# Kernel optimization log

Measured on AMD Instinct MI355X. Metric: run time of the kernel, lower is better.

## Reference

```python
import jax, jax.numpy as jnp
import numpy as np

B, N, N_IN, N_H = 8192, 16, 512, 256
NEG_ROUND = 1
MARGIN = 0.5
EPS = 1e-6  # torch F.pairwise_distance default eps


def setup_inputs() -> dict:
    key = jax.random.key(0)
    k0, k1, k2, k3 = jax.random.split(key, 4)
    seq1 = jax.random.normal(k0, (B, N, N_IN), dtype=jnp.float32)
    adj = jax.random.uniform(k1, (B, N, N), dtype=jnp.float32)
    # GCN linear (bias=False), xavier_uniform on [n_h, n_in] == same bound for [n_in, n_h]
    gx = float(np.sqrt(6.0 / (N_IN + N_H)))
    W_gcn = jax.random.uniform(k2, (N_IN, N_H), dtype=jnp.float32, minval=-gx, maxval=gx)
    b_gcn = jnp.zeros((N_H,), dtype=jnp.float32)  # Simple_GCN self.bias, init 0
    prelu_a = jnp.asarray(0.25, dtype=jnp.float32)  # nn.PReLU default
    bx = float(np.sqrt(6.0 / (N_H + N_H)))
    W_bil = jax.random.uniform(k3, (N_H, N_H), dtype=jnp.float32, minval=-bx, maxval=bx)
    b_bil = jnp.zeros((), dtype=jnp.float32)
    return {"seq1": seq1, "adj": adj, "W_gcn": W_gcn, "b_gcn": b_gcn,
            "prelu_a": prelu_a, "W_bil": W_bil, "b_bil": b_bil}


def reference(seq1, adj, W_gcn, b_gcn, prelu_a, W_bil, b_bil):
    # Simple_GCN: linear -> adjacency aggregate -> bias -> PReLU
    seq_fts = jnp.einsum('bnf,fh->bnh', seq1, W_gcn)           # [B,N,n_h]
    h1 = jnp.einsum('bnm,bmh->bnh', adj, seq_fts) + b_gcn      # bmm(adj, seq_fts)+bias
    h1 = jnp.where(h1 >= 0, h1, prelu_a * h1)                  # PReLU

    # avg readout over context nodes; last node is the target
    c = jnp.mean(h1[:, :-1, :], axis=1)                        # [B,n_h]
    h_mv = h1[:, -1, :]                                        # [B,n_h]

    def bilinear(x1, x2):  # nn.Bilinear(n_h, n_h, 1)
        return jnp.einsum('bi,ij,bj->b', x1, W_bil, x2)[:, None] + b_bil  # [B,1]

    scs = [bilinear(h_mv, c)]
    c_mi = c
    for _ in range(NEG_ROUND):  # fixed small loop, mirrors torch shift
        c_mi = jnp.concatenate([c_mi[-2:-1, :], c_mi[:-1, :]], axis=0)
        scs.append(bilinear(h_mv, c_mi))

    pos_dis = jnp.linalg.norm(h_mv - c + EPS, axis=-1)         # F.pairwise_distance
    neg_dis = jnp.linalg.norm(h_mv - c_mi + EPS, axis=-1)

    logits = jnp.concatenate(scs, axis=0)                      # [(1+NEG)*B, 1]
    # MarginRankingLoss(margin, reduction='none') with y=-1:
    # max(0, -y*(x1-x2)+margin) = max(0, (pos-neg)+margin)
    loss2 = jnp.maximum(0.0, (pos_dis - neg_dis) + MARGIN)     # [B]
    return (logits, loss2)
```

## Files before the change

kernel.cpp:

```cpp
#include <hip/hip_runtime.h>
#include <stdint.h>

typedef float f32x4 __attribute__((ext_vector_type(4)));
typedef __bf16 bfrag __attribute__((ext_vector_type(8)));
typedef unsigned short us4 __attribute__((ext_vector_type(4)));

__device__ __forceinline__ unsigned short f2bf(float f) {
  unsigned u = __float_as_uint(f);
  u += 0x7fff + ((u >> 16) & 1);
  return (unsigned short)(u >> 16);
}
__device__ __forceinline__ float bf2f(unsigned short s) {
  return __uint_as_float(((unsigned)s) << 16);
}

typedef __attribute__((address_space(3))) void lds_vp;
typedef __attribute__((address_space(1))) void gl_vp;
__device__ __forceinline__ void gload16(const void* g, void* l) {
  __builtin_amdgcn_global_load_lds((const gl_vp*)g, (lds_vp*)l, 16, 0, 0);
}

__global__ __launch_bounds__(256)
void conv_w_k(const float* __restrict__ Wg, const float* __restrict__ Wb,
              unsigned short* __restrict__ WgT, unsigned short* __restrict__ WbT) {
  int i = blockIdx.x * 256 + threadIdx.x;
  if (i < 512 * 256) { int k = i >> 8, c = i & 255; WgT[c * 512 + k] = f2bf(Wg[i]); }
  if (i < 256 * 256) { int k = i >> 8, c = i & 255; WbT[c * 256 + k] = f2bf(Wb[i]); }
}

__device__ __forceinline__ void stage1(const float* __restrict__ A,
                                       const unsigned short* __restrict__ Bt,
                                       char* buf, int tile, int kc, int t) {
#pragma unroll
  for (int i = 0; i < 4; i++) {
    int c = i * 512 + t;
    int row = c >> 4, s = c & 15;
    int sp = s ^ (row & 7);
    gload16(A + (size_t)(tile * 128 + row) * 512 + kc * 64 + sp * 4, buf + c * 16);
  }
#pragma unroll
  for (int i = 0; i < 4; i++) {
    int c = i * 512 + t;
    int col = c >> 3, s = c & 7;
    int sp = s ^ (col & 7);
    gload16(Bt + (size_t)col * 512 + kc * 64 + sp * 8, buf + 32768 + c * 16);
  }
}

__global__ __launch_bounds__(512)
void fused1_k(const float* __restrict__ A, const unsigned short* __restrict__ Bt,
              const float* __restrict__ adj, const float* __restrict__ b_gcn,
              const float* __restrict__ prelu_a,
              float* __restrict__ Cout, float* __restrict__ Hmv) {
  extern __shared__ __align__(16) char sm[];
  const int t = threadIdx.x;
  const int lane = t & 63;
  const int wid = t >> 6;
  const int wm = wid >> 2, wn = wid & 3;
  const int lrow = lane & 15, lgrp = lane >> 4;
  const int wg = blockIdx.x;

  const float pa = prelu_a[0];
  const f32x4 bg = *(const f32x4*)(b_gcn + lane * 4);

  stage1(A, Bt, sm, wg * 4, 0, t);

  for (int mt = 0; mt < 4; ++mt) {
    const int tile = wg * 4 + mt;
    f32x4 acc[4][4];
#pragma unroll
    for (int m = 0; m < 4; m++)
#pragma unroll
      for (int n = 0; n < 4; n++) acc[m][n] = (f32x4)0.0f;

    for (int kc = 0; kc < 8; ++kc) {
      char* cur = sm + (kc & 1) * 65536;
      if (!(mt == 3 && kc == 7)) {
        int nt = (kc < 7) ? tile : tile + 1;
        int nk = (kc < 7) ? kc + 1 : 0;
        stage1(A, Bt, sm + ((kc + 1) & 1) * 65536, nt, nk, t);
        asm volatile("s_waitcnt vmcnt(8)" ::: "memory");
      } else {
        asm volatile("s_waitcnt vmcnt(0)" ::: "memory");
      }
      __builtin_amdgcn_s_barrier();
      asm volatile("" ::: "memory");

#pragma unroll
      for (int kk = 0; kk < 2; kk++) {
        bfrag bfv[4];
#pragma unroll
        for (int n = 0; n < 4; n++) {
          int bcol = wn * 64 + n * 16 + lrow;
          int gs = (kk * 4 + lgrp) ^ (bcol & 7);
          bfv[n] = *(const bfrag*)(cur + 32768 + bcol * 128 + (gs << 4));
        }
#pragma unroll
        for (int m = 0; m < 4; m++) {
          int arow = wm * 64 + m * 16 + lrow;
          int s0 = (kk * 8 + lgrp * 2) ^ (arow & 7);
          int s1 = (kk * 8 + lgrp * 2 + 1) ^ (arow & 7);
          f32x4 lo = *(const f32x4*)(cur + arow * 256 + (s0 << 4));
          f32x4 hi = *(const f32x4*)(cur + arow * 256 + (s1 << 4));
          bfrag am;
          am[0] = (__bf16)lo.x; am[1] = (__bf16)lo.y; am[2] = (__bf16)lo.z; am[3] = (__bf16)lo.w;
          am[4] = (__bf16)hi.x; am[5] = (__bf16)hi.y; am[6] = (__bf16)hi.z; am[7] = (__bf16)hi.w;
#pragma unroll
          for (int n = 0; n < 4; n++)
            acc[m][n] = __builtin_amdgcn_mfma_f32_16x16x32_bf16(am, bfv[n], acc[m][n], 0, 0, 0);
        }
      }
      __builtin_amdgcn_s_barrier();
      asm volatile("" ::: "memory");
    }

    unsigned short* sf = (unsigned short*)(sm + 65536);
#pragma unroll
    for (int m = 0; m < 4; m++) {
      int row = wm * 64 + m * 16 + lgrp * 4;
#pragma unroll
      for (int n = 0; n < 4; n++) {
        int col = wn * 64 + n * 16 + lrow;
#pragma unroll
        for (int rr = 0; rr < 4; rr++)
          sf[(row + rr) * 256 + col] = f2bf(acc[m][n][rr]);
      }
    }
    asm volatile("s_waitcnt lgkmcnt(0)" ::: "memory");
    __builtin_amdgcn_s_barrier();
    asm volatile("" ::: "memory");

    f32x4 sfr[16];
#pragma unroll
    for (int mm = 0; mm < 16; mm++) {
      us4 q = *(const us4*)(sf + (wid * 16 + mm) * 256 + lane * 4);
      f32x4 v;
      v.x = bf2f(q.x); v.y = bf2f(q.y); v.z = bf2f(q.z); v.w = bf2f(q.w);
      sfr[mm] = v;
    }
    const int b = tile * 8 + wid;
    const float* adjb = adj + (size_t)b * 256;
    f32x4 cacc = (f32x4)0.0f;
    f32x4 hmv = (f32x4)0.0f;
#pragma unroll
    for (int n = 0; n < 16; n++) {
      f32x4 a4 = (f32x4)0.0f;
#pragma unroll
      for (int m = 0; m < 16; m++) a4 += adjb[n * 16 + m] * sfr[m];
      a4 += bg;
      f32x4 hv;
      hv.x = a4.x >= 0.f ? a4.x : pa * a4.x;
      hv.y = a4.y >= 0.f ? a4.y : pa * a4.y;
      hv.z = a4.z >= 0.f ? a4.z : pa * a4.z;
      hv.w = a4.w >= 0.f ? a4.w : pa * a4.w;
      if (n < 15) cacc += hv; else hmv = hv;
    }
    cacc *= (1.0f / 15.0f);
    *(f32x4*)(Cout + (size_t)b * 256 + lane * 4) = cacc;
    *(f32x4*)(Hmv + (size_t)b * 256 + lane * 4) = hmv;

    asm volatile("s_waitcnt lgkmcnt(0)" ::: "memory");
    __builtin_amdgcn_s_barrier();
    asm volatile("" ::: "memory");
  }
}

__device__ __forceinline__ void stage2(const float* __restrict__ A,
                                       const unsigned short* __restrict__ Bt,
                                       char* buf, int wg, int kc, int t) {
  {
    int c = t & 255;
    int row = c >> 3, s = c & 7;
    int sp = s ^ (((row & 3) << 1) | ((row >> 2) & 1));
    gload16(A + (size_t)(wg * 32 + row) * 256 + kc * 32 + sp * 4, buf + c * 16);
  }
#pragma unroll
  for (int i = 0; i < 2; i++) {
    int c = i * 512 + t;
    int col = c >> 2, s = c & 3;
    int sp = s ^ ((col ^ (col >> 2)) & 3);
    gload16(Bt + (size_t)col * 256 + kc * 32 + sp * 8, buf + 4096 + c * 16);
  }
}

__global__ __launch_bounds__(512)
void fused2_k(const float* __restrict__ A, const unsigned short* __restrict__ Bt,
              const float* __restrict__ C, const float* __restrict__ Hmv,
              const float* __restrict__ b_bil, float* __restrict__ out) {
  __shared__ __align__(16) char sm2[40960];
  const int t = threadIdx.x;
  const int lane = t & 63;
  const int wid = t >> 6;
  const int wm = wid >> 2, wn = wid & 3;
  const int lrow = lane & 15, lgrp = lane >> 4;
  const int wg = blockIdx.x;

  f32x4 acc[4];
#pragma unroll
  for (int n = 0; n < 4; n++) acc[n] = (f32x4)0.0f;

  stage2(A, Bt, sm2, wg, 0, t);

  for (int kc = 0; kc < 8; ++kc) {
    char* cur = sm2 + (kc & 1) * 20480;
    if (kc + 1 < 8) {
      stage2(A, Bt, sm2 + ((kc + 1) & 1) * 20480, wg, kc + 1, t);
      asm volatile("s_waitcnt vmcnt(3)" ::: "memory");
    } else {
      asm volatile("s_waitcnt vmcnt(0)" ::: "memory");
    }
    __builtin_amdgcn_s_barrier();
    asm volatile("" ::: "memory");

    bfrag bf[4];
#pragma unroll
    for (int n = 0; n < 4; n++) {
      int bcol = wn * 64 + n * 16 + lrow;
      int sB = (bcol ^ (bcol >> 2)) & 3;
      bf[n] = *(const bfrag*)(cur + 4096 + bcol * 64 + ((lgrp ^ sB) << 4));
    }
    {
      int arow = wm * 16 + lrow;
      int sw = ((arow & 3) << 1) | ((arow >> 2) & 1);
      f32x4 lo = *(const f32x4*)(cur + arow * 128 + (((lgrp * 2) ^ sw) << 4));
      f32x4 hi = *(const f32x4*)(cur + arow * 128 + (((lgrp * 2 + 1) ^ sw) << 4));
      bfrag am;
      am[0] = (__bf16)lo.x; am[1] = (__bf16)lo.y; am[2] = (__bf16)lo.z; am[3] = (__bf16)lo.w;
      am[4] = (__bf16)hi.x; am[5] = (__bf16)hi.y; am[6] = (__bf16)hi.z; am[7] = (__bf16)hi.w;
#pragma unroll
      for (int n = 0; n < 4; n++)
        acc[n] = __builtin_amdgcn_mfma_f32_16x16x32_bf16(am, bf[n], acc[n], 0, 0, 0);
    }
    __builtin_amdgcn_s_barrier();
    asm volatile("" ::: "memory");
  }

  float* sf = (float*)sm2;
  {
    int row = wm * 16 + lgrp * 4;
#pragma unroll
    for (int n = 0; n < 4; n++) {
      int col = wn * 64 + n * 16 + lrow;
#pragma unroll
      for (int rr = 0; rr < 4; rr++)
        sf[(row + rr) * 256 + col] = acc[n][rr];
    }
  }
  asm volatile("s_waitcnt lgkmcnt(0)" ::: "memory");
  __builtin_amdgcn_s_barrier();
  asm volatile("" ::: "memory");

  const float bb = b_bil[0];
#pragma unroll
  for (int r = 0; r < 4; ++r) {
    const int row = wid * 4 + r;
    const int b = wg * 32 + row;
    const int bp = (b == 0) ? 8190 : (b - 1);
    f32x4 tv = *(const f32x4*)(sf + row * 256 + lane * 4);
    f32x4 cv = *(const f32x4*)(C + (size_t)b * 256 + lane * 4);
    f32x4 cp = *(const f32x4*)(C + (size_t)bp * 256 + lane * 4);
    f32x4 hv = *(const f32x4*)(Hmv + (size_t)b * 256 + lane * 4);
    f32x4 d0 = hv - cv + 1e-6f;
    f32x4 d1 = hv - cp + 1e-6f;
    float s0 = tv.x * cv.x + tv.y * cv.y + tv.z * cv.z + tv.w * cv.w;
    float s1 = tv.x * cp.x + tv.y * cp.y + tv.z * cp.z + tv.w * cp.w;
    float p = d0.x * d0.x + d0.y * d0.y + d0.z * d0.z + d0.w * d0.w;
    float q = d1.x * d1.x + d1.y * d1.y + d1.z * d1.z + d1.w * d1.w;
#pragma unroll
    for (int m = 1; m < 64; m <<= 1) {
      s0 += __shfl_xor(s0, m, 64);
      s1 += __shfl_xor(s1, m, 64);
      p  += __shfl_xor(p, m, 64);
      q  += __shfl_xor(q, m, 64);
    }
    if (lane == 0) {
      out[b] = s0 + bb;
      out[8192 + b] = s1 + bb;
      out[16384 + b] = fmaxf(0.0f, sqrtf(p) - sqrtf(q) + 0.5f);
    }
  }
}

extern "C" void kernel_launch(void* const* d_in, const int* in_sizes, int n_in,
                              void* d_out, int out_size, void* d_ws, size_t ws_size,
                              hipStream_t stream) {
  (void)in_sizes; (void)n_in; (void)out_size; (void)ws_size;
  const float* seq1 = (const float*)d_in[0];
  const float* adj  = (const float*)d_in[1];
  const float* Wg   = (const float*)d_in[2];
  const float* bg   = (const float*)d_in[3];
  const float* pa   = (const float*)d_in[4];
  const float* Wb   = (const float*)d_in[5];
  const float* bb   = (const float*)d_in[6];
  float* out = (float*)d_out;
  char* ws = (char*)d_ws;

  unsigned short* WgT = (unsigned short*)(ws);
  unsigned short* WbT = (unsigned short*)(ws + 262144);
  float* C   = (float*)(ws + 524288);
  float* HMV = (float*)(ws + 524288 + 8388608);

  (void)hipFuncSetAttribute((const void*)fused1_k,
                            hipFuncAttributeMaxDynamicSharedMemorySize, 131072);

  hipLaunchKernelGGL(conv_w_k, dim3(512), dim3(256), 0, stream, Wg, Wb, WgT, WbT);
  hipLaunchKernelGGL(fused1_k, dim3(256), dim3(512), 131072, stream,
                     seq1, WgT, adj, bg, pa, C, HMV);
  hipLaunchKernelGGL(fused2_k, dim3(256), dim3(512), 0, stream,
                     HMV, WbT, C, HMV, bb, out);
}
```

Baseline: 104.8 us.

## Replace LDS-staged persistent GEMM with direct global loads and more blocks

The first fused kernel no longer stages seq1 and the transposed GCN weight through double-buffered LDS with async global-to-LDS loads. Each wave now reads its MFMA fragments straight from global memory. The kernel processes one 128-row tile per block over 1024 blocks instead of looping over four tiles per block, and uses only a 64KB static LDS buffer for the aggregation step. The goal is higher occupancy and less barrier and LDS traffic, relying on caches for operand reuse. The cost is that the global fragment loads are strided and uncoalesced, and the copy-compute overlap of the explicit pipeline is lost.

```diff
diff --git a/kernel.cpp b/kernel.cpp
--- a/kernel.cpp
+++ b/kernel.cpp
@@ -28,31 +28,12 @@
   if (i < 256 * 256) { int k = i >> 8, c = i & 255; WbT[c * 256 + k] = f2bf(Wb[i]); }
 }
 
-__device__ __forceinline__ void stage1(const float* __restrict__ A,
-                                       const unsigned short* __restrict__ Bt,
-                                       char* buf, int tile, int kc, int t) {
-#pragma unroll
-  for (int i = 0; i < 4; i++) {
-    int c = i * 512 + t;
-    int row = c >> 4, s = c & 15;
-    int sp = s ^ (row & 7);
-    gload16(A + (size_t)(tile * 128 + row) * 512 + kc * 64 + sp * 4, buf + c * 16);
-  }
-#pragma unroll
-  for (int i = 0; i < 4; i++) {
-    int c = i * 512 + t;
-    int col = c >> 3, s = c & 7;
-    int sp = s ^ (col & 7);
-    gload16(Bt + (size_t)col * 512 + kc * 64 + sp * 8, buf + 32768 + c * 16);
-  }
-}
-
-__global__ __launch_bounds__(512)
+__global__ __launch_bounds__(512, 4)
 void fused1_k(const float* __restrict__ A, const unsigned short* __restrict__ Bt,
               const float* __restrict__ adj, const float* __restrict__ b_gcn,
               const float* __restrict__ prelu_a,
               float* __restrict__ Cout, float* __restrict__ Hmv) {
-  extern __shared__ __align__(16) char sm[];
+  __shared__ unsigned short sf[128 * 256];
   const int t = threadIdx.x;
   const int lane = t & 63;
   const int wid = t >> 6;
@@ -60,109 +41,81 @@
   const int lrow = lane & 15, lgrp = lane >> 4;
   const int wg = blockIdx.x;
 
+  const float* a0 = A + (size_t)(wg * 128 + wm * 64 + lrow) * 512 + lgrp * 8;
+  const unsigned short* b0 = Bt + (size_t)(wn * 64 + lrow) * 512 + lgrp * 8;
+
+  f32x4 acc[4][4];
+#pragma unroll
+  for (int m = 0; m < 4; m++)
+#pragma unroll
+    for (int n = 0; n < 4; n++) acc[m][n] = (f32x4)0.0f;
+
+#pragma unroll 2
+  for (int kc = 0; kc < 8; ++kc) {
+#pragma unroll
+    for (int kk = 0; kk < 2; kk++) {
+      const int ko = kc * 64 + kk * 32;
+      bfrag bfv[4];
+#pragma unroll
+      for (int n = 0; n < 4; n++)
+        bfv[n] = *(const bfrag*)(b0 + (size_t)n * 16 * 512 + ko);
+#pragma unroll
+      for (int m = 0; m < 4; m++) {
+        f32x4 lo = *(const f32x4*)(a0 + (size_t)m * 16 * 512 + ko);
+        f32x4 hi = *(const f32x4*)(a0 + (size_t)m * 16 * 512 + ko + 4);
+        bfrag am;
+        am[0] = (__bf16)lo.x; am[1] = (__bf16)lo.y; am[2] = (__bf16)lo.z; am[3] = (__bf16)lo.w;
+        am[4] = (__bf16)hi.x; am[5] = (__bf16)hi.y; am[6] = (__bf16)hi.z; am[7] = (__bf16)hi.w;
+#pragma unroll
+        for (int n = 0; n < 4; n++)
+          acc[m][n] = __builtin_amdgcn_mfma_f32_16x16x32_bf16(am, bfv[n], acc[m][n], 0, 0, 0);
+      }
+    }
+  }
+
+#pragma unroll
+  for (int m = 0; m < 4; m++) {
+    int row = wm * 64 + m * 16 + lgrp * 4;
+#pragma unroll
+    for (int n = 0; n < 4; n++) {
+      int col = wn * 64 + n * 16 + lrow;
+#pragma unroll
+      for (int rr = 0; rr < 4; rr++)
+        sf[(row + rr) * 256 + col] = f2bf(acc[m][n][rr]);
+    }
+  }
+  __syncthreads();
+
   const float pa = prelu_a[0];
   const f32x4 bg = *(const f32x4*)(b_gcn + lane * 4);
-
-  stage1(A, Bt, sm, wg * 4, 0, t);
-
-  for (int mt = 0; mt < 4; ++mt) {
-    const int tile = wg * 4 + mt;
-    f32x4 acc[4][4];
-#pragma unroll
-    for (int m = 0; m < 4; m++)
-#pragma unroll
-      for (int n = 0; n < 4; n++) acc[m][n] = (f32x4)0.0f;
-
-    for (int kc = 0; kc < 8; ++kc) {
-      char* cur = sm + (kc & 1) * 65536;
-      if (!(mt == 3 && kc == 7)) {
-        int nt = (kc < 7) ? tile : tile + 1;
-        int nk = (kc < 7) ? kc + 1 : 0;
-        stage1(A, Bt, sm + ((kc + 1) & 1) * 65536, nt, nk, t);
-        asm volatile("s_waitcnt vmcnt(8)" ::: "memory");
-      } else {
-        asm volatile("s_waitcnt vmcnt(0)" ::: "memory");
-      }
-      __builtin_amdgcn_s_barrier();
-      asm volatile("" ::: "memory");
-
-#pragma unroll
-      for (int kk = 0; kk < 2; kk++) {
-        bfrag bfv[4];
-#pragma unroll
-        for (int n = 0; n < 4; n++) {
-          int bcol = wn * 64 + n * 16 + lrow;
-          int gs = (kk * 4 + lgrp) ^ (bcol & 7);
-          bfv[n] = *(const bfrag*)(cur + 32768 + bcol * 128 + (gs << 4));
-        }
-#pragma unroll
-        for (int m = 0; m < 4; m++) {
-          int arow = wm * 64 + m * 16 + lrow;
-          int s0 = (kk * 8 + lgrp * 2) ^ (arow & 7);
-          int s1 = (kk * 8 + lgrp * 2 + 1) ^ (arow & 7);
-          f32x4 lo = *(const f32x4*)(cur + arow * 256 + (s0 << 4));
-          f32x4 hi = *(const f32x4*)(cur + arow * 256 + (s1 << 4));
-          bfrag am;
-          am[0] = (__bf16)lo.x; am[1] = (__bf16)lo.y; am[2] = (__bf16)lo.z; am[3] = (__bf16)lo.w;
-          am[4] = (__bf16)hi.x; am[5] = (__bf16)hi.y; am[6] = (__bf16)hi.z; am[7] = (__bf16)hi.w;
-#pragma unroll
-          for (int n = 0; n < 4; n++)
-            acc[m][n] = __builtin_amdgcn_mfma_f32_16x16x32_bf16(am, bfv[n], acc[m][n], 0, 0, 0);
-        }
-      }
-      __builtin_amdgcn_s_barrier();
-      asm volatile("" ::: "memory");
-    }
-
-    unsigned short* sf = (unsigned short*)(sm + 65536);
-#pragma unroll
-    for (int m = 0; m < 4; m++) {
-      int row = wm * 64 + m * 16 + lgrp * 4;
-#pragma unroll
-      for (int n = 0; n < 4; n++) {
-        int col = wn * 64 + n * 16 + lrow;
-#pragma unroll
-        for (int rr = 0; rr < 4; rr++)
-          sf[(row + rr) * 256 + col] = f2bf(acc[m][n][rr]);
-      }
-    }
-    asm volatile("s_waitcnt lgkmcnt(0)" ::: "memory");
-    __builtin_amdgcn_s_barrier();
-    asm volatile("" ::: "memory");
-
-    f32x4 sfr[16];
-#pragma unroll
-    for (int mm = 0; mm < 16; mm++) {
-      us4 q = *(const us4*)(sf + (wid * 16 + mm) * 256 + lane * 4);
-      f32x4 v;
-      v.x = bf2f(q.x); v.y = bf2f(q.y); v.z = bf2f(q.z); v.w = bf2f(q.w);
-      sfr[mm] = v;
-    }
-    const int b = tile * 8 + wid;
-    const float* adjb = adj + (size_t)b * 256;
-    f32x4 cacc = (f32x4)0.0f;
-    f32x4 hmv = (f32x4)0.0f;
-#pragma unroll
-    for (int n = 0; n < 16; n++) {
-      f32x4 a4 = (f32x4)0.0f;
-#pragma unroll
-      for (int m = 0; m < 16; m++) a4 += adjb[n * 16 + m] * sfr[m];
-      a4 += bg;
-      f32x4 hv;
-      hv.x = a4.x >= 0.f ? a4.x : pa * a4.x;
-      hv.y = a4.y >= 0.f ? a4.y : pa * a4.y;
-      hv.z = a4.z >= 0.f ? a4.z : pa * a4.z;
-      hv.w = a4.w >= 0.f ? a4.w : pa * a4.w;
-      if (n < 15) cacc += hv; else hmv = hv;
-    }
-    cacc *= (1.0f / 15.0f);
-    *(f32x4*)(Cout + (size_t)b * 256 + lane * 4) = cacc;
-    *(f32x4*)(Hmv + (size_t)b * 256 + lane * 4) = hmv;
-
-    asm volatile("s_waitcnt lgkmcnt(0)" ::: "memory");
-    __builtin_amdgcn_s_barrier();
-    asm volatile("" ::: "memory");
-  }
+  f32x4 sfr[16];
+#pragma unroll
+  for (int mm = 0; mm < 16; mm++) {
+    us4 q = *(const us4*)(sf + (wid * 16 + mm) * 256 + lane * 4);
+    f32x4 v;
+    v.x = bf2f(q.x); v.y = bf2f(q.y); v.z = bf2f(q.z); v.w = bf2f(q.w);
+    sfr[mm] = v;
+  }
+  const int b = wg * 8 + wid;
+  const float* adjb = adj + (size_t)b * 256;
+  f32x4 cacc = (f32x4)0.0f;
+  f32x4 hmv = (f32x4)0.0f;
+#pragma unroll
+  for (int n = 0; n < 16; n++) {
+    f32x4 a4 = (f32x4)0.0f;
+#pragma unroll
+    for (int m = 0; m < 16; m++) a4 += adjb[n * 16 + m] * sfr[m];
+    a4 += bg;
+    f32x4 hv;
+    hv.x = a4.x >= 0.f ? a4.x : pa * a4.x;
+    hv.y = a4.y >= 0.f ? a4.y : pa * a4.y;
+    hv.z = a4.z >= 0.f ? a4.z : pa * a4.z;
+    hv.w = a4.w >= 0.f ? a4.w : pa * a4.w;
+    if (n < 15) cacc += hv; else hmv = hv;
+  }
+  cacc *= (1.0f / 15.0f);
+  *(f32x4*)(Cout + (size_t)b * 256 + lane * 4) = cacc;
+  *(f32x4*)(Hmv + (size_t)b * 256 + lane * 4) = hmv;
 }
 
 __device__ __forceinline__ void stage2(const float* __restrict__ A,
@@ -300,11 +253,8 @@
   float* C   = (float*)(ws + 524288);
   float* HMV = (float*)(ws + 524288 + 8388608);
 
-  (void)hipFuncSetAttribute((const void*)fused1_k,
-                            hipFuncAttributeMaxDynamicSharedMemorySize, 131072);
-
   hipLaunchKernelGGL(conv_w_k, dim3(512), dim3(256), 0, stream, Wg, Wb, WgT, WbT);
-  hipLaunchKernelGGL(fused1_k, dim3(256), dim3(512), 131072, stream,
+  hipLaunchKernelGGL(fused1_k, dim3(1024), dim3(512), 0, stream,
                      seq1, WgT, adj, bg, pa, C, HMV);
   hipLaunchKernelGGL(fused2_k, dim3(256), dim3(512), 0, stream,
                      HMV, WbT, C, HMV, bb, out);
```

Measured after the change: 227.1 us. +116.7%, slower.
